# Performance work log

Hardware: AMD Instinct MI355X
Metric: run time of the kernel (lower is better)

Reference implementation:

```python
import jax, jax.numpy as jnp
import numpy as np

N_NODES = 100000
N_EDGES = 1200000
N_GRAPHS = 128
D_IN = 64
D_HID = 64
N_CLASSES = 10


def gcn_conv(x, row, col, W, b):
    """PyG GCNConv: h = x@W; add self-loops; sym-norm deg^-1/2 gather-scatter; + bias."""
    n = x.shape[0]
    h = x @ W  # [N, out]
    loop = jnp.arange(n)
    r = jnp.concatenate([row, loop])
    c = jnp.concatenate([col, loop])
    deg = jax.ops.segment_sum(jnp.ones_like(c, dtype=x.dtype), c, num_segments=n)
    dinv = jax.lax.rsqrt(jnp.maximum(deg, 1.0))  # with self-loops deg >= 1
    norm = dinv[r] * dinv[c]  # [E+N]
    msg = h[r] * norm[:, None]  # gather + per-edge scale
    out = jax.ops.segment_sum(msg, c, num_segments=n)  # scatter-add at targets
    return out + b


def global_mean_pool(x, batch, num_graphs):
    s = jax.ops.segment_sum(x, batch, num_segments=num_graphs)
    cnt = jax.ops.segment_sum(jnp.ones((x.shape[0],), dtype=x.dtype), batch, num_segments=num_graphs)
    return s / jnp.maximum(cnt, 1.0)[:, None]


def setup_inputs() -> dict:
    key = jax.random.key(0)
    ks = jax.random.split(key, 12)
    x = jax.random.normal(ks[0], (N_NODES, D_IN), dtype=jnp.float32)
    edge_index = jax.random.randint(ks[1], (2, N_EDGES), 0, N_NODES, dtype=jnp.int64)
    batch = jnp.sort(jax.random.randint(ks[2], (N_NODES,), 0, N_GRAPHS, dtype=jnp.int64))

    def glorot(k, fan_in, fan_out):
        lim = (6.0 / (fan_in + fan_out)) ** 0.5
        return jax.random.uniform(k, (fan_in, fan_out), jnp.float32, -lim, lim)

    return {
        "x": x,
        "edge_index": edge_index,
        "batch": batch,
        "W1": glorot(ks[3], D_IN, D_HID),
        "b1": jnp.zeros((D_HID,), jnp.float32),
        "W2": glorot(ks[4], D_HID, D_HID),
        "b2": jnp.zeros((D_HID,), jnp.float32),
        "W3": glorot(ks[5], D_HID, D_HID),
        "b3": jnp.zeros((D_HID,), jnp.float32),
        "linW": glorot(ks[6], D_HID, N_CLASSES),
        "linb": jnp.zeros((N_CLASSES,), jnp.float32),
    }


def reference(x, edge_index, batch, W1, b1, W2, b2, W3, b3, linW, linb):
    row, col = edge_index[0], edge_index[1]
    h = jax.nn.relu(gcn_conv(x, row, col, W1, b1))
    h = jax.nn.relu(gcn_conv(h, row, col, W2, b2))
    h = gcn_conv(h, row, col, W3, b3)
    g = global_mean_pool(h, batch, N_GRAPHS)  # [B, hidden]
    # dropout p=0.5 is identity in eval mode (training=False)
    return g @ linW + linb  # [B, num_classes]
```

## Files before the change

kernel.cpp:

```cpp
#include <hip/hip_runtime.h>
#include <hip/hip_bf16.h>


#define N_NODES 100000
#define N_EDGES 1200000
#define N_GRAPHS 128
#define D 64
#define N_CLASSES 10

#define NB 512
#define BSZ 196
#define PEB 4096
#define PEB4 (PEB/4)

typedef unsigned short ushort_t;

__device__ __forceinline__ float bf2f(ushort_t u) {
    union { unsigned int i; float f; } v;
    v.i = ((unsigned int)u) << 16;
    return v.f;
}
__device__ __forceinline__ ushort_t f2bf(float f) {
    __hip_bfloat16 hb = __float2bfloat16(f);
    return *(ushort_t*)&hb;
}

__global__ void init_k(int* __restrict__ bcount,
                       float* __restrict__ gsum, float* __restrict__ cnt) {
    int i = blockIdx.x * 256 + threadIdx.x;
    if (i < NB) bcount[i] = 0;
    if (i < N_GRAPHS * D) gsum[i] = 0.0f;
    if (i < N_GRAPHS) cnt[i] = 0.0f;
}

__global__ void count_k(const int4* __restrict__ col4, int* __restrict__ bcount,
                        const int* __restrict__ batch, float* __restrict__ cnt,
                        int E4, int n) {
    __shared__ int h[NB];
    __shared__ int bh[N_GRAPHS];
    for (int i = threadIdx.x; i < NB; i += 256) h[i] = 0;
    if (threadIdx.x < N_GRAPHS) bh[threadIdx.x] = 0;
    __syncthreads();
    int base = blockIdx.x * PEB4;
#pragma unroll
    for (int k = 0; k < 4; ++k) {
        int idx = base + k * 256 + threadIdx.x;
        if (idx < E4) {
            int4 c = col4[idx];
            atomicAdd(&h[c.x / BSZ], 1);
            atomicAdd(&h[c.y / BSZ], 1);
            atomicAdd(&h[c.z / BSZ], 1);
            atomicAdd(&h[c.w / BSZ], 1);
        }
    }
    for (int i = blockIdx.x * 256 + threadIdx.x; i < n; i += gridDim.x * 256)
        atomicAdd(&bh[batch[i]], 1);
    __syncthreads();
    for (int i = threadIdx.x; i < NB; i += 256)
        if (h[i]) atomicAdd(&bcount[i], h[i]);
    if (threadIdx.x < N_GRAPHS && bh[threadIdx.x])
        atomicAdd(&cnt[threadIdx.x], (float)bh[threadIdx.x]);
}

__global__ void scan_k(const int* __restrict__ bcount, int* __restrict__ bstart,
                       int* __restrict__ bcursor) {
    __shared__ int s[NB];
    int t = threadIdx.x;
    int v0 = bcount[t];
    s[t] = v0;
    __syncthreads();
    for (int off = 1; off < NB; off <<= 1) {
        int v = (t >= off) ? s[t - off] : 0;
        __syncthreads();
        s[t] += v;
        __syncthreads();
    }
    int ex = s[t] - v0;
    bstart[t] = ex;
    bcursor[t] = ex;
}

__global__ void scatter_k(const int4* __restrict__ row4, const int4* __restrict__ col4,
                          int* __restrict__ bcursor, int* __restrict__ part, int E4) {
    __shared__ int h[NB], gb[NB], c2[NB];
    for (int i = threadIdx.x; i < NB; i += 256) { h[i] = 0; c2[i] = 0; }
    __syncthreads();
    int base = blockIdx.x * PEB4;
    int4 rr[4], cc[4];
    bool ok[4];
#pragma unroll
    for (int k = 0; k < 4; ++k) {
        int idx = base + k * 256 + threadIdx.x;
        ok[k] = idx < E4;
        if (ok[k]) {
            rr[k] = row4[idx];
            cc[k] = col4[idx];
            atomicAdd(&h[cc[k].x / BSZ], 1);
            atomicAdd(&h[cc[k].y / BSZ], 1);
            atomicAdd(&h[cc[k].z / BSZ], 1);
            atomicAdd(&h[cc[k].w / BSZ], 1);
        }
    }
    __syncthreads();
    for (int i = threadIdx.x; i < NB; i += 256)
        if (h[i]) gb[i] = atomicAdd(&bcursor[i], h[i]);
    __syncthreads();
#pragma unroll
    for (int k = 0; k < 4; ++k) {
        if (ok[k]) {
            int r[4] = { rr[k].x, rr[k].y, rr[k].z, rr[k].w };
            int c[4] = { cc[k].x, cc[k].y, cc[k].z, cc[k].w };
#pragma unroll
            for (int j = 0; j < 4; ++j) {
                int bk = c[j] / BSZ;
                int dl = c[j] - bk * BSZ;
                int rk = atomicAdd(&c2[bk], 1);
                part[gb[bk] + rk] = (r[j] << 8) | dl;
            }
        }
    }
}

__global__ void sortbuild_k(const int* __restrict__ part, const int* __restrict__ bstart,
                            const int* __restrict__ bcount, int* __restrict__ csr,
                            int* __restrict__ deg, int* __restrict__ cursor,
                            float* __restrict__ dinv) {
    __shared__ int h[256], st[256], c2[256];
    int b = blockIdx.x, t = threadIdx.x;
    int ebeg = bstart[b];
    int cntE = bcount[b];
    h[t] = 0; c2[t] = 0;
    __syncthreads();
    for (int e = ebeg + t; e < ebeg + cntE; e += 256)
        atomicAdd(&h[part[e] & 255], 1);
    __syncthreads();
    int hv = h[t];
    for (int off = 1; off < 256; off <<= 1) {
        int v = (t >= off) ? h[t - off] : 0;
        __syncthreads();
        h[t] += v;
        __syncthreads();
    }
    st[t] = h[t] - hv;
    __syncthreads();
    int node = b * BSZ + t;
    if (t < BSZ && node < N_NODES) {
        deg[node] = hv;
        dinv[node] = rsqrtf((float)(hv + 1));
        cursor[node] = ebeg + st[t] + hv;
    }
    for (int e = ebeg + t; e < ebeg + cntE; e += 256) {
        int p = part[e];
        int cl = p & 255;
        int rk = atomicAdd(&c2[cl], 1);
        csr[ebeg + st[cl] + rk] = p >> 8;
    }
}

__global__ __launch_bounds__(256) void gemm_f32_k(
        const float* __restrict__ X, const float* __restrict__ W,
        const float* __restrict__ dinv, ushort_t* __restrict__ H, int n) {
    __shared__ float Xs[4][D];
    int tid = threadIdx.x, wave = tid >> 6, lane = tid & 63;
    float wcol[D];
#pragma unroll
    for (int k = 0; k < D; ++k) wcol[k] = W[k * D + lane];
    for (int row0 = blockIdx.x * 4; row0 < n; row0 += gridDim.x * 4) {
        int row = row0 + wave;
        if (row < n) {
            Xs[wave][lane] = X[(size_t)row * D + lane];
            float acc = 0.0f;
#pragma unroll
            for (int k = 0; k < D; ++k) acc += Xs[wave][k] * wcol[k];
            H[(size_t)row * D + lane] = f2bf(acc * dinv[row]);
        }
    }
}

__global__ __launch_bounds__(256) void gemm_bf16_k(
        const ushort_t* __restrict__ U, const float* __restrict__ W,
        const float* __restrict__ dinv, ushort_t* __restrict__ H, int n) {
    __shared__ float Xs[4][D];
    int tid = threadIdx.x, wave = tid >> 6, lane = tid & 63;
    float wcol[D];
#pragma unroll
    for (int k = 0; k < D; ++k) wcol[k] = W[k * D + lane];
    for (int row0 = blockIdx.x * 4; row0 < n; row0 += gridDim.x * 4) {
        int row = row0 + wave;
        if (row < n) {
            Xs[wave][lane] = fmaxf(bf2f(U[(size_t)row * D + lane]), 0.0f);
            float acc = 0.0f;
#pragma unroll
            for (int k = 0; k < D; ++k) acc += Xs[wave][k] * wcol[k];
            H[(size_t)row * D + lane] = f2bf(acc * dinv[row]);
        }
    }
}

__global__ void gather_k(const ushort_t* __restrict__ Hp, const int* __restrict__ csr,
                         const int* __restrict__ cursor, const int* __restrict__ deg,
                         const float* __restrict__ dinv, const float* __restrict__ b,
                         ushort_t* __restrict__ O, int n) {
    int c = blockIdx.x * 4 + (threadIdx.x >> 6);
    if (c >= n) return;
    int lane = threadIdx.x & 63;
    int end = cursor[c];
    int dg = deg[c];
    float acc = bf2f(Hp[(size_t)c * D + lane]);
    for (int j = end - dg; j < end; j += 64) {
        int idx = j + lane;
        int s = (idx < end) ? csr[idx] : 0;
        int cnt = min(64, end - j);
        int k = 0;
        for (; k + 4 <= cnt; k += 4) {
            int r0 = __shfl(s, k);
            int r1 = __shfl(s, k + 1);
            int r2 = __shfl(s, k + 2);
            int r3 = __shfl(s, k + 3);
            float v0 = bf2f(Hp[(size_t)r0 * D + lane]);
            float v1 = bf2f(Hp[(size_t)r1 * D + lane]);
            float v2 = bf2f(Hp[(size_t)r2 * D + lane]);
            float v3 = bf2f(Hp[(size_t)r3 * D + lane]);
            acc += v0 + v1 + v2 + v3;
        }
        for (; k < cnt; ++k) {
            int r0 = __shfl(s, k);
            acc += bf2f(Hp[(size_t)r0 * D + lane]);
        }
    }
    O[(size_t)c * D + lane] = f2bf(b[lane] + dinv[c] * acc);
}

#define POOL_CHUNK 64
__global__ void pool_k(const ushort_t* __restrict__ H, const int* __restrict__ batch,
                       float* __restrict__ gsum, int n) {
    int wid = blockIdx.x * 4 + (threadIdx.x >> 6);
    int lane = threadIdx.x & 63;
    int start = wid * POOL_CHUNK;
    if (start >= n) return;
    int m = min(POOL_CHUNK, n - start);
    int bv = batch[min(start + lane, n - 1)];
    int cur = __shfl(bv, 0);
    float acc = 0.0f;
    for (int k = 0; k < m; ++k) {
        int bb = __shfl(bv, k);
        if (bb != cur) {
            atomicAdd(&gsum[cur * D + lane], acc);
            cur = bb; acc = 0.0f;
        }
        acc += bf2f(H[(size_t)(start + k) * D + lane]);
    }
    atomicAdd(&gsum[cur * D + lane], acc);
}

__global__ void final_k(const float* __restrict__ gsum, const float* __restrict__ cnt,
                        const float* __restrict__ linW, const float* __restrict__ linb,
                        float* __restrict__ out) {
    int tid = blockIdx.x * 256 + threadIdx.x;
    if (tid >= N_GRAPHS * N_CLASSES) return;
    int b = tid / N_CLASSES, c = tid % N_CLASSES;
    float inv = 1.0f / fmaxf(cnt[b], 1.0f);
    float acc = linb[c];
#pragma unroll
    for (int k = 0; k < D; ++k)
        acc += gsum[b * D + k] * inv * linW[k * N_CLASSES + c];
    out[tid] = acc;
}

extern "C" void kernel_launch(void* const* d_in, const int* in_sizes, int n_in,
                              void* d_out, int out_size, void* d_ws, size_t ws_size,
                              hipStream_t stream) {
    const float* x    = (const float*)d_in[0];
    const int*   ei   = (const int*)  d_in[1];
    const int*   batch= (const int*)  d_in[2];
    const float* W1   = (const float*)d_in[3];
    const float* b1   = (const float*)d_in[4];
    const float* W2   = (const float*)d_in[5];
    const float* b2   = (const float*)d_in[6];
    const float* W3   = (const float*)d_in[7];
    const float* b3   = (const float*)d_in[8];
    const float* linW = (const float*)d_in[9];
    const float* linb = (const float*)d_in[10];
    float* out = (float*)d_out;

    const int N = N_NODES, E = N_EDGES, E4 = N_EDGES / 4;
    const int4* row4 = (const int4*)ei;
    const int4* col4 = (const int4*)(ei + E);

    int* wsi = (int*)d_ws;
    float* dinv   = (float*)wsi;
    int*   deg    = wsi + 100352;
    int*   cursor = deg + 100352;
    int*   csr    = cursor + 100352;
    int*   part   = csr + 1200128;
    int*   bcount = part + 1200128;
    int*   bstart = bcount + 512;
    int*   bcursor= bstart + 512;
    ushort_t* bufH = (ushort_t*)(bcursor + 512);
    ushort_t* bufA = bufH + (size_t)N * D;
    float* gsum   = (float*)(bufA + (size_t)N * D);
    float* cnt    = gsum + N_GRAPHS * D;

    const int nb_part  = (E + PEB - 1) / PEB;
    const int nb_gather= (N + 3) / 4;
    const int nb_gemm  = 2048;
    const int nwaves   = (N + POOL_CHUNK - 1) / POOL_CHUNK;
    const int nb_pool  = (nwaves + 3) / 4;

    init_k<<<(N_GRAPHS * D + 255) / 256, 256, 0, stream>>>(bcount, gsum, cnt);
    count_k<<<nb_part, 256, 0, stream>>>(col4, bcount, batch, cnt, E4, N);
    scan_k<<<1, NB, 0, stream>>>(bcount, bstart, bcursor);
    scatter_k<<<nb_part, 256, 0, stream>>>(row4, col4, bcursor, part, E4);
    sortbuild_k<<<NB, 256, 0, stream>>>(part, bstart, bcount, csr, deg, cursor, dinv);

    gemm_f32_k<<<nb_gemm, 256, 0, stream>>>(x, W1, dinv, bufH, N);
    gather_k<<<nb_gather, 256, 0, stream>>>(bufH, csr, cursor, deg, dinv, b1, bufA, N);
    gemm_bf16_k<<<nb_gemm, 256, 0, stream>>>(bufA, W2, dinv, bufH, N);
    gather_k<<<nb_gather, 256, 0, stream>>>(bufH, csr, cursor, deg, dinv, b2, bufA, N);
    gemm_bf16_k<<<nb_gemm, 256, 0, stream>>>(bufA, W3, dinv, bufH, N);
    gather_k<<<nb_gather, 256, 0, stream>>>(bufH, csr, cursor, deg, dinv, b3, bufA, N);

    pool_k<<<nb_pool, 256, 0, stream>>>(bufA, batch, gsum, N);
    final_k<<<(N_GRAPHS * N_CLASSES + 255) / 256, 256, 0, stream>>>(gsum, cnt, linW, linb, out);
}
```

Measured before the change: 364.8 us.

## Drop init kernel, use per-block histograms, unroll gather and split GEMM accumulators

Removes the separate init kernel by having count_k write per-block histogram slices that scan_k sums, with scan_k also zeroing gsum and cnt. Graph node counts move from count_k into pool_k, which adds run lengths per segment. The gather loop is unrolled to 8 loads with a tree reduction to expose more memory-level parallelism. The GEMM inner products use two accumulators to shorten the dependency chain. These cut a launch and global atomics in exchange for a serial 293-block sum inside the single-block scan.

```diff
diff --git a/kernel.cpp b/kernel.cpp
--- a/kernel.cpp
+++ b/kernel.cpp
@@ -12,6 +12,7 @@
 #define BSZ 196
 #define PEB 4096
 #define PEB4 (PEB/4)
+#define NBP ((N_EDGES + PEB - 1) / PEB)
 
 typedef unsigned short ushort_t;
 
@@ -25,21 +26,9 @@
     return *(ushort_t*)&hb;
 }
 
-__global__ void init_k(int* __restrict__ bcount,
-                       float* __restrict__ gsum, float* __restrict__ cnt) {
-    int i = blockIdx.x * 256 + threadIdx.x;
-    if (i < NB) bcount[i] = 0;
-    if (i < N_GRAPHS * D) gsum[i] = 0.0f;
-    if (i < N_GRAPHS) cnt[i] = 0.0f;
-}
-
-__global__ void count_k(const int4* __restrict__ col4, int* __restrict__ bcount,
-                        const int* __restrict__ batch, float* __restrict__ cnt,
-                        int E4, int n) {
+__global__ void count_k(const int4* __restrict__ col4, int* __restrict__ hist, int E4) {
     __shared__ int h[NB];
-    __shared__ int bh[N_GRAPHS];
     for (int i = threadIdx.x; i < NB; i += 256) h[i] = 0;
-    if (threadIdx.x < N_GRAPHS) bh[threadIdx.x] = 0;
     __syncthreads();
     int base = blockIdx.x * PEB4;
 #pragma unroll
@@ -53,20 +42,19 @@
             atomicAdd(&h[c.w / BSZ], 1);
         }
     }
-    for (int i = blockIdx.x * 256 + threadIdx.x; i < n; i += gridDim.x * 256)
-        atomicAdd(&bh[batch[i]], 1);
-    __syncthreads();
-    for (int i = threadIdx.x; i < NB; i += 256)
-        if (h[i]) atomicAdd(&bcount[i], h[i]);
-    if (threadIdx.x < N_GRAPHS && bh[threadIdx.x])
-        atomicAdd(&cnt[threadIdx.x], (float)bh[threadIdx.x]);
-}
-
-__global__ void scan_k(const int* __restrict__ bcount, int* __restrict__ bstart,
-                       int* __restrict__ bcursor) {
+    __syncthreads();
+    int* slice = hist + (size_t)blockIdx.x * NB;
+    for (int i = threadIdx.x; i < NB; i += 256) slice[i] = h[i];
+}
+
+__global__ void scan_k(const int* __restrict__ hist, int* __restrict__ bcount,
+                       int* __restrict__ bstart, int* __restrict__ bcursor,
+                       float* __restrict__ gsum, float* __restrict__ cnt) {
     __shared__ int s[NB];
     int t = threadIdx.x;
-    int v0 = bcount[t];
+    int v0 = 0;
+    for (int blk = 0; blk < NBP; ++blk) v0 += hist[(size_t)blk * NB + t];
+    bcount[t] = v0;
     s[t] = v0;
     __syncthreads();
     for (int off = 1; off < NB; off <<= 1) {
@@ -78,6 +66,8 @@
     int ex = s[t] - v0;
     bstart[t] = ex;
     bcursor[t] = ex;
+    for (int i = t; i < N_GRAPHS * D; i += NB) gsum[i] = 0.0f;
+    if (t < N_GRAPHS) cnt[t] = 0.0f;
 }
 
 __global__ void scatter_k(const int4* __restrict__ row4, const int4* __restrict__ col4,
@@ -169,10 +159,13 @@
         int row = row0 + wave;
         if (row < n) {
             Xs[wave][lane] = X[(size_t)row * D + lane];
-            float acc = 0.0f;
-#pragma unroll
-            for (int k = 0; k < D; ++k) acc += Xs[wave][k] * wcol[k];
-            H[(size_t)row * D + lane] = f2bf(acc * dinv[row]);
+            float a0 = 0.0f, a1 = 0.0f;
+#pragma unroll
+            for (int k = 0; k < D; k += 2) {
+                a0 += Xs[wave][k] * wcol[k];
+                a1 += Xs[wave][k + 1] * wcol[k + 1];
+            }
+            H[(size_t)row * D + lane] = f2bf((a0 + a1) * dinv[row]);
         }
     }
 }
@@ -189,10 +182,13 @@
         int row = row0 + wave;
         if (row < n) {
             Xs[wave][lane] = fmaxf(bf2f(U[(size_t)row * D + lane]), 0.0f);
-            float acc = 0.0f;
-#pragma unroll
-            for (int k = 0; k < D; ++k) acc += Xs[wave][k] * wcol[k];
-            H[(size_t)row * D + lane] = f2bf(acc * dinv[row]);
+            float a0 = 0.0f, a1 = 0.0f;
+#pragma unroll
+            for (int k = 0; k < D; k += 2) {
+                a0 += Xs[wave][k] * wcol[k];
+                a1 += Xs[wave][k + 1] * wcol[k + 1];
+            }
+            H[(size_t)row * D + lane] = f2bf((a0 + a1) * dinv[row]);
         }
     }
 }
@@ -210,20 +206,25 @@
     for (int j = end - dg; j < end; j += 64) {
         int idx = j + lane;
         int s = (idx < end) ? csr[idx] : 0;
-        int cnt = min(64, end - j);
+        int m = min(64, end - j);
         int k = 0;
-        for (; k + 4 <= cnt; k += 4) {
+        for (; k + 8 <= m; k += 8) {
+            float v[8];
+#pragma unroll
+            for (int p = 0; p < 8; ++p) {
+                int r = __shfl(s, k + p);
+                v[p] = bf2f(Hp[(size_t)r * D + lane]);
+            }
+            acc += ((v[0] + v[1]) + (v[2] + v[3])) + ((v[4] + v[5]) + (v[6] + v[7]));
+        }
+        for (; k + 2 <= m; k += 2) {
             int r0 = __shfl(s, k);
             int r1 = __shfl(s, k + 1);
-            int r2 = __shfl(s, k + 2);
-            int r3 = __shfl(s, k + 3);
             float v0 = bf2f(Hp[(size_t)r0 * D + lane]);
             float v1 = bf2f(Hp[(size_t)r1 * D + lane]);
-            float v2 = bf2f(Hp[(size_t)r2 * D + lane]);
-            float v3 = bf2f(Hp[(size_t)r3 * D + lane]);
-            acc += v0 + v1 + v2 + v3;
-        }
-        for (; k < cnt; ++k) {
+            acc += v0 + v1;
+        }
+        if (k < m) {
             int r0 = __shfl(s, k);
             acc += bf2f(Hp[(size_t)r0 * D + lane]);
         }
@@ -233,7 +234,7 @@
 
 #define POOL_CHUNK 64
 __global__ void pool_k(const ushort_t* __restrict__ H, const int* __restrict__ batch,
-                       float* __restrict__ gsum, int n) {
+                       float* __restrict__ gsum, float* __restrict__ cnt, int n) {
     int wid = blockIdx.x * 4 + (threadIdx.x >> 6);
     int lane = threadIdx.x & 63;
     int start = wid * POOL_CHUNK;
@@ -242,15 +243,19 @@
     int bv = batch[min(start + lane, n - 1)];
     int cur = __shfl(bv, 0);
     float acc = 0.0f;
+    int run = 0;
     for (int k = 0; k < m; ++k) {
         int bb = __shfl(bv, k);
         if (bb != cur) {
             atomicAdd(&gsum[cur * D + lane], acc);
-            cur = bb; acc = 0.0f;
+            if (lane == 0) atomicAdd(&cnt[cur], (float)run);
+            cur = bb; acc = 0.0f; run = 0;
         }
         acc += bf2f(H[(size_t)(start + k) * D + lane]);
+        ++run;
     }
     atomicAdd(&gsum[cur * D + lane], acc);
+    if (lane == 0) atomicAdd(&cnt[cur], (float)run);
 }
 
 __global__ void final_k(const float* __restrict__ gsum, const float* __restrict__ cnt,
@@ -293,7 +298,8 @@
     int*   cursor = deg + 100352;
     int*   csr    = cursor + 100352;
     int*   part   = csr + 1200128;
-    int*   bcount = part + 1200128;
+    int*   hist   = part + 1200128;
+    int*   bcount = hist + NBP * NB;
     int*   bstart = bcount + 512;
     int*   bcursor= bstart + 512;
     ushort_t* bufH = (ushort_t*)(bcursor + 512);
@@ -301,16 +307,14 @@
     float* gsum   = (float*)(bufA + (size_t)N * D);
     float* cnt    = gsum + N_GRAPHS * D;
 
-    const int nb_part  = (E + PEB - 1) / PEB;
     const int nb_gather= (N + 3) / 4;
     const int nb_gemm  = 2048;
     const int nwaves   = (N + POOL_CHUNK - 1) / POOL_CHUNK;
     const int nb_pool  = (nwaves + 3) / 4;
 
-    init_k<<<(N_GRAPHS * D + 255) / 256, 256, 0, stream>>>(bcount, gsum, cnt);
-    count_k<<<nb_part, 256, 0, stream>>>(col4, bcount, batch, cnt, E4, N);
-    scan_k<<<1, NB, 0, stream>>>(bcount, bstart, bcursor);
-    scatter_k<<<nb_part, 256, 0, stream>>>(row4, col4, bcursor, part, E4);
+    count_k<<<NBP, 256, 0, stream>>>(col4, hist, E4);
+    scan_k<<<1, NB, 0, stream>>>(hist, bcount, bstart, bcursor, gsum, cnt);
+    scatter_k<<<NBP, 256, 0, stream>>>(row4, col4, bcursor, part, E4);
     sortbuild_k<<<NB, 256, 0, stream>>>(part, bstart, bcount, csr, deg, cursor, dinv);
 
     gemm_f32_k<<<nb_gemm, 256, 0, stream>>>(x, W1, dinv, bufH, N);
@@ -320,6 +324,6 @@
     gemm_bf16_k<<<nb_gemm, 256, 0, stream>>>(bufA, W3, dinv, bufH, N);
     gather_k<<<nb_gather, 256, 0, stream>>>(bufH, csr, cursor, deg, dinv, b3, bufA, N);
 
-    pool_k<<<nb_pool, 256, 0, stream>>>(bufA, batch, gsum, N);
+    pool_k<<<nb_pool, 256, 0, stream>>>(bufA, batch, gsum, cnt, N);
     final_k<<<(N_GRAPHS * N_CLASSES + 255) / 256, 256, 0, stream>>>(gsum, cnt, linW, linb, out);
 }
```

Measured after the change: 386.0 us. 1.06x slower.
